# Kernel tuning notes

Measured on AMD Instinct MI355X. Metric: run time of the kernel, lower is better.

## Reference

```python
import jax, jax.numpy as jnp
import numpy as np

B, T, F_DIM, H = 4096, 64, 128, 128
LAM = 0.5  # lambda_spurious

def _gelu(x):
    return jax.nn.gelu(x, approximate=False)  # torch nn.GELU default = exact erf

def _ln(x, g, b):
    m = x.mean(-1, keepdims=True)
    v = ((x - m) ** 2).mean(-1, keepdims=True)
    return (x - m) / jnp.sqrt(v + 1e-5) * g + b

def _lin_init(k, fan_in, fan_out):
    kw, kb = jax.random.split(k)
    s = 1.0 / np.sqrt(fan_in)
    w = jax.random.uniform(kw, (fan_in, fan_out), minval=-s, maxval=s, dtype=jnp.float32)
    b = jax.random.uniform(kb, (fan_out,), minval=-s, maxval=s, dtype=jnp.float32)
    return w, b

def setup_inputs() -> dict:
    key = jax.random.key(0)
    ks = jax.random.split(key, 16)
    inp = {}
    inp['causal_summary'] = jax.random.normal(ks[0], (B, T, F_DIM), dtype=jnp.float32)
    inp['spurious_summary'] = jax.random.normal(ks[1], (B, T, F_DIM), dtype=jnp.float32)
    inp['labels'] = jax.random.randint(ks[2], (B,), 0, 2)
    inp['valid_mask'] = jax.random.bernoulli(ks[3], 0.7, (B, T))
    inp['ce_w1'], inp['ce_b1'] = _lin_init(ks[4], F_DIM, H)
    inp['ce_w2'], inp['ce_b2'] = _lin_init(ks[5], H, H)
    inp['se_w1'], inp['se_b1'] = _lin_init(ks[6], F_DIM, H)
    inp['se_w2'], inp['se_b2'] = _lin_init(ks[7], H, H)
    inp['cd_g'] = jnp.ones((H,), jnp.float32); inp['cd_b'] = jnp.zeros((H,), jnp.float32)
    inp['cd_w1'], inp['cd_b1'] = _lin_init(ks[8], H, H)
    inp['cd_w2'], inp['cd_b2'] = _lin_init(ks[9], H, 2)
    inp['jd_g'] = jnp.ones((2 * H,), jnp.float32); inp['jd_b'] = jnp.zeros((2 * H,), jnp.float32)
    inp['jd_w1'], inp['jd_b1'] = _lin_init(ks[10], 2 * H, H)
    inp['jd_w2'], inp['jd_b2'] = _lin_init(ks[11], H, 2)
    return inp

def _forward(causal_summary, spurious_summary, labels, valid_mask, params):
    (ce_w1, ce_b1, ce_w2, ce_b2, se_w1, se_b1, se_w2, se_b2,
     cd_g, cd_b, cd_w1, cd_b1, cd_w2, cd_b2,
     jd_g, jd_b, jd_w1, jd_b1, jd_w2, jd_b2) = params
    enc = lambda x, w1, b1, w2, b2: _gelu(x @ w1 + b1) @ w2 + b2
    c_rep = enc(causal_summary, ce_w1, ce_b1, ce_w2, ce_b2)    # [B,T,H]
    s_rep = enc(spurious_summary, se_w1, se_b1, se_w2, se_b2)  # [B,T,H]
    dec = lambda x, g, b, w1, b1, w2, b2: _gelu(_ln(x, g, b) @ w1 + b1) @ w2 + b2
    logits_c = dec(c_rep, cd_g, cd_b, cd_w1, cd_b1, cd_w2, cd_b2)  # [B,T,2]
    logits_j = dec(jnp.concatenate([c_rep, s_rep], -1), jd_g, jd_b, jd_w1, jd_b1, jd_w2, jd_b2)
    onehot = jax.nn.one_hot(labels, 2, dtype=jnp.float32)      # [B,2]
    # per-sample cross entropy: logsumexp - logit[label]
    ce_c = jax.nn.logsumexp(logits_c, -1) - jnp.einsum('btk,bk->bt', logits_c, onehot)
    ce_j = jax.nn.logsumexp(logits_j, -1) - jnp.einsum('btk,bk->bt', logits_j, onehot)
    mask_f = valid_mask.astype(jnp.float32)                    # [B,T]
    counts = jnp.einsum('bt,bk->tk', mask_f, onehot)           # per-step active label counts
    tot = counts.sum(-1)                                       # [T]
    probs = counts / jnp.clip(tot, 1.0, None)[:, None]
    ent = -(probs * jnp.log(probs + 1e-8)).sum(-1)             # [T] label entropy per step
    step_valid = (tot >= 2.0).astype(jnp.float32)              # torch skips steps with active.sum() < 2
    mi_c = ent[None, :] - ce_c                                 # mutual information estimate
    cond = jnp.maximum(ce_c - ce_j, 0.0)                       # == clamp(mi_joint - mi_c, 0)
    reward = mask_f * step_valid[None, :] * (mi_c - LAM * cond)
    denom = jnp.clip(tot, 1.0, None)
    aux_step = 0.5 * ((mask_f * ce_c).sum(0) + (mask_f * ce_j).sum(0)) / denom  # mean of (aux_c, aux_joint)
    n_valid = step_valid.sum()
    aux_loss = jnp.where(n_valid > 0, (step_valid * aux_step).sum() / jnp.maximum(n_valid, 1.0), 0.0)
    return reward, aux_loss

def reference(causal_summary, spurious_summary, labels, valid_mask,
              ce_w1, ce_b1, ce_w2, ce_b2, se_w1, se_b1, se_w2, se_b2,
              cd_g, cd_b, cd_w1, cd_b1, cd_w2, cd_b2,
              jd_g, jd_b, jd_w1, jd_b1, jd_w2, jd_b2):
    params = (ce_w1, ce_b1, ce_w2, ce_b2, se_w1, se_b1, se_w2, se_b2,
              cd_g, cd_b, cd_w1, cd_b1, cd_w2, cd_b2,
              jd_g, jd_b, jd_w1, jd_b1, jd_w2, jd_b2)
    return _forward(causal_summary, spurious_summary, labels, valid_mask, params)
```

## Files before the change

### kernel.cpp

```cpp
#include <hip/hip_runtime.h>
#include <hip/hip_fp16.h>

#define B_ 4096
#define T_ 64
#define NROWS (B_*T_)
#define BLOB_B 2099200
#define PIMG_B (BLOB_B + 7*32768)

typedef _Float16 f16x8 __attribute__((ext_vector_type(8)));
typedef float    f32x4 __attribute__((ext_vector_type(4)));

__device__ __forceinline__ float gelu_f(float x){
    float u = 0.7978845608028654f * (x + 0.044715f * x * x * x);
    float t = 1.f - 2.f / (__expf(2.f * u) + 1.f);
    return 0.5f * x * (1.f + t);
}

__device__ __forceinline__ void gll16(const void* g, void* l){
    __builtin_amdgcn_global_load_lds(
        (const __attribute__((address_space(1))) void*)g,
        (__attribute__((address_space(3))) void*)l, 16, 0, 0);
}

__device__ __forceinline__ void stage_w(const char* gsrc, char* wbuf, int wave, int lane){
    const char* g = gsrc + wave * 8192 + lane * 16;
    char* l = wbuf + wave * 8192;
#pragma unroll
    for (int r = 0; r < 8; r++) gll16(g + r * 1024, l + r * 1024);
}

__device__ __forceinline__ void stage_p(const char* gsrc, char* sp, int wave, int lane){
    gll16(gsrc + wave * 1024 + lane * 16, sp + wave * 1024);
}

__device__ __forceinline__ void load_in(f16x8* a, const float* __restrict__ p, int g){
#pragma unroll
    for (int ks = 0; ks < 4; ks++){
        const float* q = p + ks * 32 + g * 8;
        float4 v0 = *(const float4*)q, v1 = *(const float4*)(q + 4);
        f16x8 t;
        t[0]=(_Float16)v0.x; t[1]=(_Float16)v0.y; t[2]=(_Float16)v0.z; t[3]=(_Float16)v0.w;
        t[4]=(_Float16)v1.x; t[5]=(_Float16)v1.y; t[6]=(_Float16)v1.z; t[7]=(_Float16)v1.w;
        a[ks] = t;
    }
}

__device__ __forceinline__ void load_a(f16x8* a, const char* ab, int c, int g){
    const int rswz = (c & 7) << 4;
    const char* rp = ab + c * 256;
#pragma unroll
    for (int ks = 0; ks < 4; ks++)
        a[ks] = *(const f16x8*)(rp + ((ks * 64 + g * 16) ^ rswz));
}

__device__ __forceinline__ void mfma_tile(f32x4* acc, const f16x8* a,
                                          const unsigned short* wb, int c, int g){
#pragma unroll
    for (int n = 0; n < 8; n++){
        const int r = n * 16 + c;
        const char* rp = (const char*)wb + r * 256;
        const int swz = (r & 7) << 4;
#pragma unroll
        for (int ks = 0; ks < 4; ks++){
            f16x8 b = *(const f16x8*)(rp + ((ks * 64 + g * 16) ^ swz));
            acc[n] = __builtin_amdgcn_mfma_f32_16x16x32_f16(a[ks], b, acc[n], 0, 0, 0);
        }
    }
}

template<bool GELU>
__device__ __forceinline__ void epi_store(const f32x4* acc, char* ab,
                                          const unsigned short* sbh, int boff, int c, int g){
    const _Float16* sbf = (const _Float16*)sbh;
#pragma unroll
    for (int n = 0; n < 8; n++){
        const int col = n * 16 + c;
        float bi = (float)sbf[boff + col];
#pragma unroll
        for (int rr = 0; rr < 4; rr++){
            float v = acc[n][rr] + bi;
            if (GELU) v = gelu_f(v);
            int row = g * 4 + rr;
            *(_Float16*)(ab + row * 256 + ((col << 1) ^ ((row & 7) << 4))) = (_Float16)v;
        }
    }
}

__device__ __forceinline__ void build_y(f16x8* y, const f16x8* x, float mu, float rs,
                                        const unsigned short* sbh, int goff, int boff, int g){
#pragma unroll
    for (int ks = 0; ks < 4; ks++){
        f16x8 gam = *(const f16x8*)((const char*)sbh + goff * 2 + ks * 64 + g * 16);
        f16x8 bet = *(const f16x8*)((const char*)sbh + boff * 2 + ks * 64 + g * 16);
        f16x8 t;
#pragma unroll
        for (int j = 0; j < 8; j++){
            float v = ((float)x[ks][j] - mu) * rs * (float)gam[j] + (float)bet[j];
            t[j] = (_Float16)v;
        }
        y[ks] = t;
    }
}

__device__ __forceinline__ void row_stats(const f16x8* x, float& s0, float& s1){
    s0 = 0.f; s1 = 0.f;
#pragma unroll
    for (int ks = 0; ks < 4; ks++)
#pragma unroll
        for (int j = 0; j < 8; j++){ float v = (float)x[ks][j]; s0 += v; s1 += v*v; }
    s0 += __shfl_xor(s0, 16); s0 += __shfl_xor(s0, 32);
    s1 += __shfl_xor(s1, 16); s1 += __shfl_xor(s1, 32);
}

__device__ __forceinline__ void logits_ce(const f32x4* acc, const unsigned short* sbh,
                                          int b1off, int w2off, const float* __restrict__ b2,
                                          int c, int g, int lab, float* ce){
    const _Float16* sbf = (const _Float16*)sbh;
    float l0[4] = {0,0,0,0}, l1[4] = {0,0,0,0};
#pragma unroll
    for (int n = 0; n < 8; n++){
        const int r = n * 16 + c;
        float b1v = (float)sbf[b1off + r];
        float wx  = (float)sbf[w2off + 2 * r];
        float wy  = (float)sbf[w2off + 2 * r + 1];
#pragma unroll
        for (int rr = 0; rr < 4; rr++){
            float hv = gelu_f(acc[n][rr] + b1v);
            l0[rr] += hv * wx; l1[rr] += hv * wy;
        }
    }
    const float b2x = b2[0], b2y = b2[1];
#pragma unroll
    for (int rr = 0; rr < 4; rr++){
#pragma unroll
        for (int m = 1; m < 16; m <<= 1){ l0[rr] += __shfl_xor(l0[rr], m); l1[rr] += __shfl_xor(l1[rr], m); }
        float v0 = l0[rr] + b2x, v1 = l1[rr] + b2y;
        float mx = fmaxf(v0, v1);
        float lse = mx + logf(expf(v0 - mx) + expf(v1 - mx));
        ce[rr] = lse - (lab ? v1 : v0);
    }
}

__global__ void k_prep(const float* __restrict__ ce_w1, const float* __restrict__ ce_w2,
                       const float* __restrict__ se_w1, const float* __restrict__ se_w2,
                       const float* __restrict__ cd_w1, const float* __restrict__ jd_w1,
                       const float* __restrict__ ce_b1, const float* __restrict__ ce_b2,
                       const float* __restrict__ se_b1, const float* __restrict__ se_b2,
                       const float* __restrict__ cd_g,  const float* __restrict__ cd_bt,
                       const float* __restrict__ cd_b1, const float* __restrict__ jd_g,
                       const float* __restrict__ jd_bt, const float* __restrict__ jd_b1,
                       const float* __restrict__ cd_w2, const float* __restrict__ jd_w2,
                       const int* __restrict__ mask, const int* __restrict__ labels,
                       float* __restrict__ ws){
    char* blob = (char*)ws + BLOB_B;
    const int bid = blockIdx.x, tid = threadIdx.x;
    if (bid < 448){
        int e = bid * 256 + tid;
        int m = e >> 14, idx = e & 16383;
        int k = idx >> 7, cc = idx & 127;
        const float* src;
        switch (m){
            case 0: src = ce_w1; break;
            case 1: src = ce_w2; break;
            case 2: src = se_w1; break;
            case 3: src = se_w2; break;
            case 4: src = cd_w1; break;
            case 5: src = jd_w1; break;
            default: src = jd_w1 + 128 * 128; break;
        }
        float v = src[k * 128 + cc];
        int byte = m * 32768 + cc * 256 + ((k << 1) ^ ((cc & 7) << 4));
        *(_Float16*)(blob + byte) = (_Float16)v;
    } else if (bid < 512){
        int t = bid - 448;
        float c0 = 0.f, c1 = 0.f;
        for (int b = tid; b < B_; b += 256){
            if (mask[b * T_ + t]){
                if (labels[b] == 1) c1 += 1.f; else c0 += 1.f;
            }
        }
        for (int m = 1; m < 64; m <<= 1){ c0 += __shfl_xor(c0, m); c1 += __shfl_xor(c1, m); }
        __shared__ float sh[8];
        int w = tid >> 6, l = tid & 63;
        if (l == 0){ sh[w] = c0; sh[4 + w] = c1; }
        __syncthreads();
        if (tid == 0){
            float a0 = sh[0] + sh[1] + sh[2] + sh[3];
            float a1 = sh[4] + sh[5] + sh[6] + sh[7];
            float tot = a0 + a1;
            float d = fmaxf(tot, 1.f);
            float p0 = a0 / d, p1 = a1 / d;
            float ent = -(p0 * logf(p0 + 1e-8f) + p1 * logf(p1 + 1e-8f));
            ws[t] = ent;
            ws[64 + t] = (tot >= 2.f) ? 1.f : 0.f;
            ws[128 + t] = tot;
        }
    } else {
        _Float16* p = (_Float16*)((char*)ws + PIMG_B);
        if (tid < 128){
            p[tid]       = (_Float16)ce_b1[tid]; p[128 + tid] = (_Float16)ce_b2[tid];
            p[256 + tid] = (_Float16)se_b1[tid]; p[384 + tid] = (_Float16)se_b2[tid];
            p[512 + tid] = (_Float16)cd_g[tid];  p[640 + tid] = (_Float16)cd_bt[tid];
            p[768 + tid] = (_Float16)cd_b1[tid]; p[896 + tid] = (_Float16)jd_b1[tid];
        } else {
            int i = tid - 128;
            p[1024 + i] = (_Float16)jd_g[i];        p[1152 + i] = (_Float16)jd_g[128 + i];
            p[1280 + i] = (_Float16)jd_bt[i];       p[1408 + i] = (_Float16)jd_bt[128 + i];
            p[1536 + 2*i] = (_Float16)cd_w2[2*i];   p[1537 + 2*i] = (_Float16)cd_w2[2*i+1];
            p[1792 + 2*i] = (_Float16)jd_w2[2*i];   p[1793 + 2*i] = (_Float16)jd_w2[2*i+1];
        }
    }
}

__global__ __launch_bounds__(256, 2) void k_main(
    const float* __restrict__ xc, const float* __restrict__ xs,
    const int* __restrict__ labels, const int* __restrict__ mask,
    const float* __restrict__ cd_b2, const float* __restrict__ jd_b2,
    float* __restrict__ ws, float* __restrict__ out)
{
    __shared__ __align__(16) unsigned short wbuf[128 * 128];
    __shared__ __align__(16) unsigned short abuf[4 * 16 * 128];
    __shared__ __align__(16) unsigned short sp[2048];

    const int tid = threadIdx.x;
    const int wave = tid >> 6, lane = tid & 63;
    const int c = lane & 15, g = lane >> 4;
    const int wrow0 = blockIdx.x * 64 + wave * 16;
    char* const ab = (char*)abuf + wave * 4096;
    const int lab = labels[(wrow0 + g * 4) >> 6];
    const char* blob = (const char*)ws + BLOB_B;

    f16x8 aX[4], a4[4], cr[4], sr[4], yb[4];
    f32x4 acc[8];
    float ceC[4], ceJ[4];
    float s0c, s1c, mcv, rcv, jmv, jrv;

    stage_p((const char*)ws + PIMG_B, (char*)sp, wave, lane);
    stage_w(blob + 0 * 32768, (char*)wbuf, wave, lane);
    load_in(aX, xc + (wrow0 + c) * 128, g);
    __syncthreads();

#pragma unroll
    for (int n = 0; n < 8; n++) acc[n] = (f32x4){0.f,0.f,0.f,0.f};
    mfma_tile(acc, aX, wbuf, c, g);
    __syncthreads();
    stage_w(blob + 1 * 32768, (char*)wbuf, wave, lane);
    epi_store<true>(acc, ab, sp, 0, c, g);
    __syncthreads();

    load_a(a4, ab, c, g);
#pragma unroll
    for (int n = 0; n < 8; n++) acc[n] = (f32x4){0.f,0.f,0.f,0.f};
    mfma_tile(acc, a4, wbuf, c, g);
    __syncthreads();
    stage_w(blob + 2 * 32768, (char*)wbuf, wave, lane);
    epi_store<false>(acc, ab, sp, 128, c, g);
    load_in(aX, xs + (wrow0 + c) * 128, g);
    __syncthreads();

    load_a(cr, ab, c, g);
#pragma unroll
    for (int n = 0; n < 8; n++) acc[n] = (f32x4){0.f,0.f,0.f,0.f};
    mfma_tile(acc, aX, wbuf, c, g);
    __syncthreads();
    stage_w(blob + 3 * 32768, (char*)wbuf, wave, lane);
    epi_store<true>(acc, ab, sp, 256, c, g);
    row_stats(cr, s0c, s1c);
    __syncthreads();

    load_a(a4, ab, c, g);
#pragma unroll
    for (int n = 0; n < 8; n++) acc[n] = (f32x4){0.f,0.f,0.f,0.f};
    mfma_tile(acc, a4, wbuf, c, g);
    __syncthreads();
    stage_w(blob + 4 * 32768, (char*)wbuf, wave, lane);
    epi_store<false>(acc, ab, sp, 384, c, g);
    __syncthreads();

    load_a(sr, ab, c, g);
    {
        float s0s, s1s;
        row_stats(sr, s0s, s1s);
        mcv = s0c * (1.f/128.f);
        rcv = rsqrtf(s1c * (1.f/128.f) - mcv * mcv + 1e-5f);
        jmv = (s0c + s0s) * (1.f/256.f);
        jrv = rsqrtf((s1c + s1s) * (1.f/256.f) - jmv * jmv + 1e-5f);
    }
    build_y(yb, cr, mcv, rcv, sp, 512, 640, g);
#pragma unroll
    for (int n = 0; n < 8; n++) acc[n] = (f32x4){0.f,0.f,0.f,0.f};
    mfma_tile(acc, yb, wbuf, c, g);
    __syncthreads();
    stage_w(blob + 5 * 32768, (char*)wbuf, wave, lane);
    logits_ce(acc, sp, 768, 1536, cd_b2, c, g, lab, ceC);
    build_y(yb, cr, jmv, jrv, sp, 1024, 1280, g);
    __syncthreads();

#pragma unroll
    for (int n = 0; n < 8; n++) acc[n] = (f32x4){0.f,0.f,0.f,0.f};
    mfma_tile(acc, yb, wbuf, c, g);
    __syncthreads();
    stage_w(blob + 6 * 32768, (char*)wbuf, wave, lane);
    build_y(yb, sr, jmv, jrv, sp, 1152, 1408, g);
    __syncthreads();

    mfma_tile(acc, yb, wbuf, c, g);
    logits_ce(acc, sp, 896, 1792, jd_b2, c, g, lab, ceJ);

    if (c == 0){
        const int rowbase = wrow0 + g * 4;
        const int4  m4 = *(const int4*)(mask + rowbase);
        const float4 e4 = *(const float4*)(ws + (rowbase & 63));
        const float4 s4 = *(const float4*)(ws + 64 + (rowbase & 63));
        const int   mm[4] = {m4.x, m4.y, m4.z, m4.w};
        const float ee[4] = {e4.x, e4.y, e4.z, e4.w};
        const float sv[4] = {s4.x, s4.y, s4.z, s4.w};
        float rw[4], mc2[4], mj2[4];
#pragma unroll
        for (int rr = 0; rr < 4; rr++){
            float mf = mm[rr] ? 1.f : 0.f;
            float cec = ceC[rr], cej = ceJ[rr];
            rw[rr]  = mf * sv[rr] * (ee[rr] - cec - 0.5f * fmaxf(cec - cej, 0.f));
            mc2[rr] = mf * cec;
            mj2[rr] = mf * cej;
        }
        *(float4*)(out + rowbase)              = (float4){rw[0], rw[1], rw[2], rw[3]};
        *(float4*)(ws + 512 + rowbase)         = (float4){mc2[0], mc2[1], mc2[2], mc2[3]};
        *(float4*)(ws + 512 + NROWS + rowbase) = (float4){mj2[0], mj2[1], mj2[2], mj2[3]};
    }
}

__global__ void k_aux1(float* __restrict__ ws){
    int t = blockIdx.x, tid = threadIdx.x;
    const float* mc = ws + 512;
    const float* mj = ws + 512 + NROWS;
    float sc = 0.f, sj = 0.f;
    for (int b = tid; b < B_; b += 256){ sc += mc[b * T_ + t]; sj += mj[b * T_ + t]; }
    for (int m = 1; m < 64; m <<= 1){ sc += __shfl_xor(sc, m); sj += __shfl_xor(sj, m); }
    __shared__ float sh[8];
    int w = tid >> 6, l = tid & 63;
    if (l == 0){ sh[w] = sc; sh[4 + w] = sj; }
    __syncthreads();
    if (tid == 0){
        float a0 = sh[0] + sh[1] + sh[2] + sh[3];
        float a1 = sh[4] + sh[5] + sh[6] + sh[7];
        ws[192 + t] = ws[64 + t] * 0.5f * (a0 + a1) / fmaxf(ws[128 + t], 1.f);
    }
}

__global__ void k_aux2(const float* __restrict__ ws, float* __restrict__ out){
    int l = threadIdx.x;
    float cv = ws[192 + l], sv = ws[64 + l];
    for (int m = 1; m < 64; m <<= 1){ cv += __shfl_xor(cv, m); sv += __shfl_xor(sv, m); }
    if (l == 0) out[NROWS] = (sv > 0.f) ? cv / fmaxf(sv, 1.f) : 0.f;
}

extern "C" void kernel_launch(void* const* d_in, const int* in_sizes, int n_in,
                              void* d_out, int out_size, void* d_ws, size_t ws_size,
                              hipStream_t stream) {
    const float* xc     = (const float*)d_in[0];
    const float* xs     = (const float*)d_in[1];
    const int*   labels = (const int*)d_in[2];
    const int*   mask   = (const int*)d_in[3];
    const float* ce_w1  = (const float*)d_in[4];
    const float* ce_b1  = (const float*)d_in[5];
    const float* ce_w2  = (const float*)d_in[6];
    const float* ce_b2  = (const float*)d_in[7];
    const float* se_w1  = (const float*)d_in[8];
    const float* se_b1  = (const float*)d_in[9];
    const float* se_w2  = (const float*)d_in[10];
    const float* se_b2  = (const float*)d_in[11];
    const float* cd_g   = (const float*)d_in[12];
    const float* cd_b   = (const float*)d_in[13];
    const float* cd_w1  = (const float*)d_in[14];
    const float* cd_b1  = (const float*)d_in[15];
    const float* cd_w2  = (const float*)d_in[16];
    const float* cd_b2  = (const float*)d_in[17];
    const float* jd_g   = (const float*)d_in[18];
    const float* jd_b   = (const float*)d_in[19];
    const float* jd_w1  = (const float*)d_in[20];
    const float* jd_b1  = (const float*)d_in[21];
    const float* jd_w2  = (const float*)d_in[22];
    const float* jd_b2  = (const float*)d_in[23];
    float* ws  = (float*)d_ws;
    float* out = (float*)d_out;

    k_prep<<<513, 256, 0, stream>>>(ce_w1, ce_w2, se_w1, se_w2, cd_w1, jd_w1,
                                    ce_b1, ce_b2, se_b1, se_b2, cd_g, cd_b,
                                    cd_b1, jd_g, jd_b, jd_b1, cd_w2, jd_w2,
                                    mask, labels, ws);
    k_main<<<4096, 256, 0, stream>>>(xc, xs, labels, mask, cd_b2, jd_b2, ws, out);
    k_aux1<<<64, 256, 0, stream>>>(ws);
    k_aux2<<<1, 64, 0, stream>>>(ws, out);
}
```

Before: 230.6 us.

## Split weight staging into halves to overlap next-layer loads with MFMA

Each 128x128 fp16 weight tile is now staged into LDS in two 64-row halves instead of one block. The next layer's first half is loaded while the MFMAs run on the current layer's second half, and its second half is loaded after the following barrier. The goal is to hide the global-to-LDS weight transfer latency behind compute, at the cost of a few extra barriers and more interleaved scheduling. It also switches the log-sum-exp to the fast __logf/__expf intrinsics and moves row_stats earlier.

```diff
diff --git a/kernel.cpp b/kernel.cpp
--- a/kernel.cpp
+++ b/kernel.cpp
@@ -22,11 +22,11 @@
         (__attribute__((address_space(3))) void*)l, 16, 0, 0);
 }
 
-__device__ __forceinline__ void stage_w(const char* gsrc, char* wbuf, int wave, int lane){
-    const char* g = gsrc + wave * 8192 + lane * 16;
-    char* l = wbuf + wave * 8192;
-#pragma unroll
-    for (int r = 0; r < 8; r++) gll16(g + r * 1024, l + r * 1024);
+__device__ __forceinline__ void stage_h(const char* gsrc, char* wbuf, int wave, int lane, int half){
+    const char* g = gsrc + half * 16384 + wave * 4096 + lane * 16;
+    char* l = wbuf + half * 16384 + wave * 4096;
+#pragma unroll
+    for (int r = 0; r < 4; r++) gll16(g + r * 1024, l + r * 1024);
 }
 
 __device__ __forceinline__ void stage_p(const char* gsrc, char* sp, int wave, int lane){
@@ -53,10 +53,10 @@
         a[ks] = *(const f16x8*)(rp + ((ks * 64 + g * 16) ^ rswz));
 }
 
-__device__ __forceinline__ void mfma_tile(f32x4* acc, const f16x8* a,
-                                          const unsigned short* wb, int c, int g){
-#pragma unroll
-    for (int n = 0; n < 8; n++){
+__device__ __forceinline__ void mfma_half(f32x4* acc, const f16x8* a,
+                                          const unsigned short* wb, int c, int g, int n0){
+#pragma unroll
+    for (int n = n0; n < n0 + 4; n++){
         const int r = n * 16 + c;
         const char* rp = (const char*)wb + r * 256;
         const int swz = (r & 7) << 4;
@@ -136,7 +136,7 @@
         for (int m = 1; m < 16; m <<= 1){ l0[rr] += __shfl_xor(l0[rr], m); l1[rr] += __shfl_xor(l1[rr], m); }
         float v0 = l0[rr] + b2x, v1 = l1[rr] + b2y;
         float mx = fmaxf(v0, v1);
-        float lse = mx + logf(expf(v0 - mx) + expf(v1 - mx));
+        float lse = mx + __logf(__expf(v0 - mx) + __expf(v1 - mx));
         ce[rr] = lse - (lab ? v1 : v0);
     }
 }
@@ -236,47 +236,56 @@
     float s0c, s1c, mcv, rcv, jmv, jrv;
 
     stage_p((const char*)ws + PIMG_B, (char*)sp, wave, lane);
-    stage_w(blob + 0 * 32768, (char*)wbuf, wave, lane);
+    stage_h(blob + 0 * 32768, (char*)wbuf, wave, lane, 0);
+    stage_h(blob + 0 * 32768, (char*)wbuf, wave, lane, 1);
     load_in(aX, xc + (wrow0 + c) * 128, g);
     __syncthreads();
 
 #pragma unroll
     for (int n = 0; n < 8; n++) acc[n] = (f32x4){0.f,0.f,0.f,0.f};
-    mfma_tile(acc, aX, wbuf, c, g);
-    __syncthreads();
-    stage_w(blob + 1 * 32768, (char*)wbuf, wave, lane);
+    mfma_half(acc, aX, wbuf, c, g, 0);
+    __syncthreads();
+    stage_h(blob + 1 * 32768, (char*)wbuf, wave, lane, 0);
+    mfma_half(acc, aX, wbuf, c, g, 4);
     epi_store<true>(acc, ab, sp, 0, c, g);
     __syncthreads();
 
+    stage_h(blob + 1 * 32768, (char*)wbuf, wave, lane, 1);
     load_a(a4, ab, c, g);
 #pragma unroll
     for (int n = 0; n < 8; n++) acc[n] = (f32x4){0.f,0.f,0.f,0.f};
-    mfma_tile(acc, a4, wbuf, c, g);
-    __syncthreads();
-    stage_w(blob + 2 * 32768, (char*)wbuf, wave, lane);
+    mfma_half(acc, a4, wbuf, c, g, 0);
+    __syncthreads();
+    stage_h(blob + 2 * 32768, (char*)wbuf, wave, lane, 0);
+    mfma_half(acc, a4, wbuf, c, g, 4);
     epi_store<false>(acc, ab, sp, 128, c, g);
     load_in(aX, xs + (wrow0 + c) * 128, g);
     __syncthreads();
 
+    stage_h(blob + 2 * 32768, (char*)wbuf, wave, lane, 1);
     load_a(cr, ab, c, g);
-#pragma unroll
-    for (int n = 0; n < 8; n++) acc[n] = (f32x4){0.f,0.f,0.f,0.f};
-    mfma_tile(acc, aX, wbuf, c, g);
-    __syncthreads();
-    stage_w(blob + 3 * 32768, (char*)wbuf, wave, lane);
+    row_stats(cr, s0c, s1c);
+#pragma unroll
+    for (int n = 0; n < 8; n++) acc[n] = (f32x4){0.f,0.f,0.f,0.f};
+    mfma_half(acc, aX, wbuf, c, g, 0);
+    __syncthreads();
+    stage_h(blob + 3 * 32768, (char*)wbuf, wave, lane, 0);
+    mfma_half(acc, aX, wbuf, c, g, 4);
     epi_store<true>(acc, ab, sp, 256, c, g);
-    row_stats(cr, s0c, s1c);
-    __syncthreads();
-
+    __syncthreads();
+
+    stage_h(blob + 3 * 32768, (char*)wbuf, wave, lane, 1);
     load_a(a4, ab, c, g);
 #pragma unroll
     for (int n = 0; n < 8; n++) acc[n] = (f32x4){0.f,0.f,0.f,0.f};
-    mfma_tile(acc, a4, wbuf, c, g);
-    __syncthreads();
-    stage_w(blob + 4 * 32768, (char*)wbuf, wave, lane);
+    mfma_half(acc, a4, wbuf, c, g, 0);
+    __syncthreads();
+    stage_h(blob + 4 * 32768, (char*)wbuf, wave, lane, 0);
+    mfma_half(acc, a4, wbuf, c, g, 4);
     epi_store<false>(acc, ab, sp, 384, c, g);
     __syncthreads();
 
+    stage_h(blob + 4 * 32768, (char*)wbuf, wave, lane, 1);
     load_a(sr, ab, c, g);
     {
         float s0s, s1s;
@@ -289,22 +298,28 @@
     build_y(yb, cr, mcv, rcv, sp, 512, 640, g);
 #pragma unroll
     for (int n = 0; n < 8; n++) acc[n] = (f32x4){0.f,0.f,0.f,0.f};
-    mfma_tile(acc, yb, wbuf, c, g);
-    __syncthreads();
-    stage_w(blob + 5 * 32768, (char*)wbuf, wave, lane);
+    mfma_half(acc, yb, wbuf, c, g, 0);
+    __syncthreads();
+    stage_h(blob + 5 * 32768, (char*)wbuf, wave, lane, 0);
+    mfma_half(acc, yb, wbuf, c, g, 4);
     logits_ce(acc, sp, 768, 1536, cd_b2, c, g, lab, ceC);
+    __syncthreads();
+
+    stage_h(blob + 5 * 32768, (char*)wbuf, wave, lane, 1);
     build_y(yb, cr, jmv, jrv, sp, 1024, 1280, g);
-    __syncthreads();
-
-#pragma unroll
-    for (int n = 0; n < 8; n++) acc[n] = (f32x4){0.f,0.f,0.f,0.f};
-    mfma_tile(acc, yb, wbuf, c, g);
-    __syncthreads();
-    stage_w(blob + 6 * 32768, (char*)wbuf, wave, lane);
+#pragma unroll
+    for (int n = 0; n < 8; n++) acc[n] = (f32x4){0.f,0.f,0.f,0.f};
+    mfma_half(acc, yb, wbuf, c, g, 0);
+    __syncthreads();
+    stage_h(blob + 6 * 32768, (char*)wbuf, wave, lane, 0);
+    mfma_half(acc, yb, wbuf, c, g, 4);
+    __syncthreads();
+
+    stage_h(blob + 6 * 32768, (char*)wbuf, wave, lane, 1);
     build_y(yb, sr, jmv, jrv, sp, 1152, 1408, g);
-    __syncthreads();
-
-    mfma_tile(acc, yb, wbuf, c, g);
+    mfma_half(acc, yb, wbuf, c, g, 0);
+    __syncthreads();
+    mfma_half(acc, yb, wbuf, c, g, 4);
     logits_ce(acc, sp, 896, 1792, jd_b2, c, g, lab, ceJ);
 
     if (c == 0){
```

New measurement: 241.0 us. +4.5%, slower.
